# Optimization experiments

Measured on AMD Instinct MI355X. Metric: run time of the kernel, lower is better.

## Reference

```python
import jax, jax.numpy as jnp
import numpy as np

B, T, D = 8, 4096, 1024

def setup_inputs() -> dict:
    key = jax.random.key(0)
    ks = jax.random.split(key, 7)
    s1 = 1.0 / np.sqrt(D)
    return {
        "x":  jax.random.normal(ks[0], (B, T, D), dtype=jnp.float32),
        "W1": jax.random.normal(ks[1], (D, D), dtype=jnp.float32) * s1,   # attn_1.weight [out,in]
        "b1": jnp.zeros((D,), dtype=jnp.float32),
        "w2": jax.random.normal(ks[2], (1, D), dtype=jnp.float32) * s1,   # attn_2.weight [1,in]
        "b2": jnp.zeros((1,), dtype=jnp.float32),
        "Wc": jax.random.normal(ks[3], (D, 2 * D), dtype=jnp.float32) * (1.0 / np.sqrt(2 * D)),
        "bc": jnp.zeros((D,), dtype=jnp.float32),
    }

def reference(x, W1, b1, w2, b2, Wc, bc):
    # additive attention scores: [B, T, 1] -> [B, T]
    h = jnp.tanh(jnp.einsum('btd,ed->bte', x, W1) + b1)
    s = (jnp.einsum('btd,od->bto', h, w2) + b2)[..., 0]          # [B, T]
    # causal prefix softmax via cumulative sums (single O(T) pass).
    # softmax is shift-invariant, so subtracting the global per-batch max is stable.
    m = jnp.max(s, axis=1, keepdims=True)                        # [B, 1]
    e = jnp.exp(s - m)                                           # [B, T]
    num = jnp.cumsum(e[..., None] * x, axis=1)                   # [B, T, D]
    den = jnp.cumsum(e, axis=1)[..., None]                       # [B, T, 1]
    ctx = num / den                                              # [B, T, D]
    combined = jnp.concatenate((ctx, x), axis=2)                 # [B, T, 2D]
    out = jnp.tanh(jnp.einsum('btk,dk->btd', combined, Wc) + bc)
    return out
```

## Files before the change

### kernel.cpp

```cpp
#include <hip/hip_runtime.h>
#include <cmath>


#define Mtot 32768
#define Dd 1024
#define Tt 4096
#define Bb 8
#define NCHUNK 64
#define TCH 64

typedef __bf16 bf16x8 __attribute__((ext_vector_type(8)));
typedef float f32x4 __attribute__((ext_vector_type(4)));

__device__ __forceinline__ unsigned short f2bf(float f) {
  unsigned int u = __float_as_uint(f);
  unsigned int r = (u + 0x7FFFu + ((u >> 16) & 1u)) >> 16;
  return (unsigned short)r;
}
__device__ __forceinline__ float bf2f(unsigned short s) {
  return __uint_as_float(((unsigned int)s) << 16);
}

__device__ __forceinline__ void gload16(const unsigned short* g, unsigned short* l) {
  __builtin_amdgcn_global_load_lds(
      (const __attribute__((address_space(1))) unsigned int*)g,
      (__attribute__((address_space(3))) unsigned int*)l, 16, 0, 0);
}

__device__ __forceinline__ void mfma_core(
    const unsigned short* __restrict__ A0, const unsigned short* __restrict__ A1,
    const unsigned short* __restrict__ W, int ldw, int Ktot,
    int m0, int n0, unsigned short* As, unsigned short* Bs, f32x4 acc[4][4]) {
  int tid = threadIdx.x;
  int lane = tid & 63, w = tid >> 6;
  int wm = w >> 1, wn = w & 1;
  int quad = lane >> 4, c = lane & 15;
  int lrow = lane >> 3;
  int col8 = (lane & 7) ^ lrow;

  for (int k0 = 0; k0 < Ktot; k0 += 64) {
    const unsigned short* Asrc = (k0 < 1024) ? A0 : A1;
    int ka = k0 & 1023;
#pragma unroll
    for (int j = 0; j < 4; ++j) {
      int row = w * 32 + j * 8 + lrow;
      gload16(Asrc + (size_t)(m0 + row) * 1024 + ka + col8 * 8, As + w * 2048 + j * 512);
      gload16(W + (size_t)(n0 + row) * ldw + k0 + col8 * 8, Bs + w * 2048 + j * 512);
    }
    __syncthreads();
#pragma unroll
    for (int ks = 0; ks < 2; ++ks) {
      bf16x8 af[4], bfr[4];
#pragma unroll
      for (int i = 0; i < 4; ++i) {
        int ra = wm * 64 + i * 16 + c;
        int pa = (ks * 4 + quad) ^ (ra & 7);
        af[i] = *(const bf16x8*)(As + ra * 64 + pa * 8);
        int rb = wn * 64 + i * 16 + c;
        int pb = (ks * 4 + quad) ^ (rb & 7);
        bfr[i] = *(const bf16x8*)(Bs + rb * 64 + pb * 8);
      }
#pragma unroll
      for (int i = 0; i < 4; ++i)
#pragma unroll
        for (int jn = 0; jn < 4; ++jn)
          acc[i][jn] = __builtin_amdgcn_mfma_f32_16x16x32_bf16(af[i], bfr[jn], acc[i][jn], 0, 0, 0);
    }
    __syncthreads();
  }
}

__global__ __launch_bounds__(256) void gemm_s(
    const unsigned short* __restrict__ xb, const unsigned short* __restrict__ W1b,
    const float* __restrict__ b1, const float* __restrict__ w2, float* __restrict__ s) {
  __shared__ unsigned short As[128 * 64];
  __shared__ unsigned short Bs[128 * 64];
  f32x4 acc[4][4];
#pragma unroll
  for (int i = 0; i < 4; ++i)
#pragma unroll
    for (int j = 0; j < 4; ++j) acc[i][j] = (f32x4){0.f, 0.f, 0.f, 0.f};
  int m0 = blockIdx.x * 128, n0 = blockIdx.y * 128;
  mfma_core(xb, xb, W1b, 1024, 1024, m0, n0, As, Bs, acc);
  int tid = threadIdx.x, lane = tid & 63, w = tid >> 6;
  int wm = w >> 1, wn = w & 1, quad = lane >> 4, c = lane & 15;
#pragma unroll
  for (int i = 0; i < 4; ++i) {
#pragma unroll
    for (int r = 0; r < 4; ++r) {
      float p = 0.f;
#pragma unroll
      for (int jn = 0; jn < 4; ++jn) {
        int n = n0 + wn * 64 + jn * 16 + c;
        p += w2[n] * tanhf(acc[i][jn][r] + b1[n]);
      }
      p += __shfl_xor(p, 1, 64);
      p += __shfl_xor(p, 2, 64);
      p += __shfl_xor(p, 4, 64);
      p += __shfl_xor(p, 8, 64);
      if (c == 0) atomicAdd(&s[m0 + wm * 64 + i * 16 + quad * 4 + r], p);
    }
  }
}

__global__ __launch_bounds__(256) void gemm_out(
    const unsigned short* __restrict__ qb, const unsigned short* __restrict__ xb,
    const unsigned short* __restrict__ Wcb, const float* __restrict__ bc_,
    float* __restrict__ out) {
  __shared__ unsigned short As[128 * 64];
  __shared__ unsigned short Bs[128 * 64];
  f32x4 acc[4][4];
#pragma unroll
  for (int i = 0; i < 4; ++i)
#pragma unroll
    for (int j = 0; j < 4; ++j) acc[i][j] = (f32x4){0.f, 0.f, 0.f, 0.f};
  int m0 = blockIdx.x * 128, n0 = blockIdx.y * 128;
  mfma_core(qb, xb, Wcb, 2048, 2048, m0, n0, As, Bs, acc);
  int tid = threadIdx.x, lane = tid & 63, w = tid >> 6;
  int wm = w >> 1, wn = w & 1, quad = lane >> 4, c = lane & 15;
#pragma unroll
  for (int i = 0; i < 4; ++i)
#pragma unroll
    for (int jn = 0; jn < 4; ++jn) {
      int n = n0 + wn * 64 + jn * 16 + c;
      float bias = bc_[n];
#pragma unroll
      for (int r = 0; r < 4; ++r) {
        int m = m0 + wm * 64 + i * 16 + quad * 4 + r;
        out[(size_t)m * Dd + n] = tanhf(acc[i][jn][r] + bias);
      }
    }
}

__global__ __launch_bounds__(256) void cast_x(const float4* __restrict__ x,
                                              ushort4* __restrict__ xb) {
  int i = blockIdx.x * 256 + threadIdx.x;
  float4 v = x[i];
  ushort4 o;
  o.x = f2bf(v.x); o.y = f2bf(v.y); o.z = f2bf(v.z); o.w = f2bf(v.w);
  xb[i] = o;
}

__global__ __launch_bounds__(256) void cast_w(
    const float* __restrict__ W1, const float* __restrict__ Wc,
    ushort4* __restrict__ W1b, ushort4* __restrict__ Wcb) {
  int i = blockIdx.x * 256 + threadIdx.x;
  if (i < 262144) {
    float4 v = ((const float4*)W1)[i];
    ushort4 o;
    o.x = f2bf(v.x); o.y = f2bf(v.y); o.z = f2bf(v.z); o.w = f2bf(v.w);
    W1b[i] = o;
  } else {
    int p = i - 262144;
    float4 v = ((const float4*)Wc)[p];
    ushort4 o;
    o.x = f2bf(v.x); o.y = f2bf(v.y); o.z = f2bf(v.z); o.w = f2bf(v.w);
    Wcb[p] = o;
  }
}

__global__ __launch_bounds__(256) void softmax_scan(
    const float* __restrict__ s, float* __restrict__ e, float* __restrict__ den) {
  int b = blockIdx.x, tid = threadIdx.x;
  const float* sb = s + (size_t)b * Tt;
  __shared__ float wsum[4], woff[4], redm[4];
  __shared__ float carry_s, total_s;
  int lane = tid & 63, wid = tid >> 6;
  float m = -1e30f;
  for (int i = tid; i < Tt; i += 256) m = fmaxf(m, sb[i]);
#pragma unroll
  for (int off = 32; off > 0; off >>= 1) m = fmaxf(m, __shfl_down(m, off, 64));
  if (lane == 0) redm[wid] = m;
  __syncthreads();
  if (tid == 0) {
    float mm = redm[0];
    for (int w = 1; w < 4; ++w) mm = fmaxf(mm, redm[w]);
    redm[0] = mm;
    carry_s = 0.f;
  }
  __syncthreads();
  m = redm[0];
  for (int c = 0; c < 16; ++c) {
    int t = c * 256 + tid;
    float v = expf(sb[t] - m);
    e[(size_t)b * Tt + t] = v;
    float sc = v;
#pragma unroll
    for (int off = 1; off < 64; off <<= 1) {
      float tt = __shfl_up(sc, off, 64);
      if (lane >= off) sc += tt;
    }
    if (lane == 63) wsum[wid] = sc;
    __syncthreads();
    if (tid == 0) {
      float a = 0.f;
      for (int w = 0; w < 4; ++w) { woff[w] = a; a += wsum[w]; }
      total_s = a;
    }
    __syncthreads();
    den[(size_t)b * Tt + t] = sc + woff[wid] + carry_s;
    __syncthreads();
    if (tid == 0) carry_s += total_s;
    __syncthreads();
  }
}

__global__ __launch_bounds__(1024) void chunk_sums(
    const unsigned short* __restrict__ xb, const float* __restrict__ e,
    float* __restrict__ S) {
  int bc = blockIdx.x;
  int b = bc >> 6, c = bc & 63;
  int d = threadIdx.x;
  const unsigned short* xp = xb + ((size_t)(b * Tt + c * TCH)) * Dd + d;
  const float* eb = e + (size_t)b * Tt + c * TCH;
  float acc = 0.f;
#pragma unroll 8
  for (int t = 0; t < TCH; ++t) acc += eb[t] * bf2f(xp[(size_t)t * Dd]);
  S[((size_t)bc) * Dd + d] = acc;
}

__global__ __launch_bounds__(256) void chunk_prefix(float* __restrict__ S) {
  int idx = blockIdx.x * 256 + threadIdx.x;
  int b = idx >> 10, d = idx & 1023;
  float* Sb = S + (size_t)b * NCHUNK * Dd + d;
  float acc = 0.f;
#pragma unroll 8
  for (int c = 0; c < NCHUNK; ++c) {
    float t = Sb[(size_t)c * Dd];
    Sb[(size_t)c * Dd] = acc;
    acc += t;
  }
}

__global__ __launch_bounds__(1024) void scan_q(
    const unsigned short* __restrict__ xb, const float* __restrict__ e,
    const float* __restrict__ den, const float* __restrict__ S,
    unsigned short* __restrict__ qb) {
  int bc = blockIdx.x;
  int b = bc >> 6, c = bc & 63;
  int d = threadIdx.x;
  int tbase = b * Tt + c * TCH;
  float acc = S[((size_t)bc) * Dd + d];
  const unsigned short* xp = xb + (size_t)tbase * Dd + d;
  const float* eb = e + tbase;
  const float* db = den + tbase;
  unsigned short* qp = qb + (size_t)tbase * Dd + d;
#pragma unroll 4
  for (int t = 0; t < TCH; ++t) {
    acc += eb[t] * bf2f(xp[(size_t)t * Dd]);
    qp[(size_t)t * Dd] = f2bf(acc / db[t]);
  }
}

extern "C" void kernel_launch(void* const* d_in, const int* in_sizes, int n_in,
                              void* d_out, int out_size, void* d_ws, size_t ws_size,
                              hipStream_t stream) {
  const float* x  = (const float*)d_in[0];
  const float* W1 = (const float*)d_in[1];
  const float* b1 = (const float*)d_in[2];
  const float* w2 = (const float*)d_in[3];
  const float* Wc = (const float*)d_in[5];
  const float* bc = (const float*)d_in[6];
  float* out = (float*)d_out;

  float* ws = (float*)d_ws;
  float* s_buf   = ws;
  float* e_buf   = ws + 32768;
  float* den_buf = ws + 65536;
  float* S_buf   = ws + 98304;
  unsigned short* qb  = (unsigned short*)(ws + 622592);
  unsigned short* xb  = (unsigned short*)(ws + 17399808);
  unsigned short* W1b = (unsigned short*)(ws + 34177024);
  unsigned short* Wcb = (unsigned short*)(ws + 34701312);

  hipMemsetAsync(s_buf, 0, (size_t)Mtot * sizeof(float), stream);

  cast_x<<<32768, 256, 0, stream>>>((const float4*)x, (ushort4*)xb);
  cast_w<<<3072, 256, 0, stream>>>(W1, Wc, (ushort4*)W1b, (ushort4*)Wcb);

  gemm_s<<<dim3(Mtot / 128, Dd / 128), 256, 0, stream>>>(xb, W1b, b1, w2, s_buf);
  softmax_scan<<<Bb, 256, 0, stream>>>(s_buf, e_buf, den_buf);
  chunk_sums<<<Bb * NCHUNK, 1024, 0, stream>>>(xb, e_buf, S_buf);
  chunk_prefix<<<Bb * Dd / 256, 256, 0, stream>>>(S_buf);
  scan_q<<<Bb * NCHUNK, 1024, 0, stream>>>(xb, e_buf, den_buf, S_buf, qb);
  gemm_out<<<dim3(Mtot / 128, Dd / 128), 256, 0, stream>>>(qb, xb, Wcb, bc, out);
}
```

Measured before the change: 579.7 us.

## Fuse cast kernels with memset, use fast tanh, and register-resident softmax scan

```diff
diff --git a/kernel.cpp b/kernel.cpp
--- a/kernel.cpp
+++ b/kernel.cpp
@@ -19,6 +19,9 @@
 }
 __device__ __forceinline__ float bf2f(unsigned short s) {
   return __uint_as_float(((unsigned int)s) << 16);
+}
+__device__ __forceinline__ float tanh_fast(float x) {
+  return 1.0f - __fdividef(2.0f, __expf(2.0f * x) + 1.0f);
 }
 
 __device__ __forceinline__ void gload16(const unsigned short* g, unsigned short* l) {
@@ -92,7 +95,7 @@
 #pragma unroll
       for (int jn = 0; jn < 4; ++jn) {
         int n = n0 + wn * 64 + jn * 16 + c;
-        p += w2[n] * tanhf(acc[i][jn][r] + b1[n]);
+        p += w2[n] * tanh_fast(acc[i][jn][r] + b1[n]);
       }
       p += __shfl_xor(p, 1, 64);
       p += __shfl_xor(p, 2, 64);
@@ -127,81 +130,86 @@
 #pragma unroll
       for (int r = 0; r < 4; ++r) {
         int m = m0 + wm * 64 + i * 16 + quad * 4 + r;
-        out[(size_t)m * Dd + n] = tanhf(acc[i][jn][r] + bias);
+        out[(size_t)m * Dd + n] = tanh_fast(acc[i][jn][r] + bias);
       }
     }
 }
 
-__global__ __launch_bounds__(256) void cast_x(const float4* __restrict__ x,
-                                              ushort4* __restrict__ xb) {
+__global__ __launch_bounds__(256) void cast_all(
+    const float4* __restrict__ x, const float4* __restrict__ W1,
+    const float4* __restrict__ Wc, ushort4* __restrict__ xb,
+    ushort4* __restrict__ W1b, ushort4* __restrict__ Wcb,
+    float4* __restrict__ s) {
   int i = blockIdx.x * 256 + threadIdx.x;
-  float4 v = x[i];
-  ushort4 o;
-  o.x = f2bf(v.x); o.y = f2bf(v.y); o.z = f2bf(v.z); o.w = f2bf(v.w);
-  xb[i] = o;
-}
-
-__global__ __launch_bounds__(256) void cast_w(
-    const float* __restrict__ W1, const float* __restrict__ Wc,
-    ushort4* __restrict__ W1b, ushort4* __restrict__ Wcb) {
-  int i = blockIdx.x * 256 + threadIdx.x;
-  if (i < 262144) {
-    float4 v = ((const float4*)W1)[i];
+  if (i < 8388608) {
+    float4 v = x[i];
     ushort4 o;
     o.x = f2bf(v.x); o.y = f2bf(v.y); o.z = f2bf(v.z); o.w = f2bf(v.w);
-    W1b[i] = o;
-  } else {
-    int p = i - 262144;
-    float4 v = ((const float4*)Wc)[p];
+    xb[i] = o;
+  } else if (i < 8650752) {
+    int p = i - 8388608;
+    float4 v = W1[p];
+    ushort4 o;
+    o.x = f2bf(v.x); o.y = f2bf(v.y); o.z = f2bf(v.z); o.w = f2bf(v.w);
+    W1b[p] = o;
+  } else if (i < 9175040) {
+    int p = i - 8650752;
+    float4 v = Wc[p];
     ushort4 o;
     o.x = f2bf(v.x); o.y = f2bf(v.y); o.z = f2bf(v.z); o.w = f2bf(v.w);
     Wcb[p] = o;
+  } else {
+    s[i - 9175040] = (float4){0.f, 0.f, 0.f, 0.f};
   }
 }
 
 __global__ __launch_bounds__(256) void softmax_scan(
     const float* __restrict__ s, float* __restrict__ e, float* __restrict__ den) {
   int b = blockIdx.x, tid = threadIdx.x;
-  const float* sb = s + (size_t)b * Tt;
-  __shared__ float wsum[4], woff[4], redm[4];
-  __shared__ float carry_s, total_s;
   int lane = tid & 63, wid = tid >> 6;
-  float m = -1e30f;
-  for (int i = tid; i < Tt; i += 256) m = fmaxf(m, sb[i]);
-#pragma unroll
-  for (int off = 32; off > 0; off >>= 1) m = fmaxf(m, __shfl_down(m, off, 64));
+  __shared__ float redm[4], wsum[4];
+  const float4* sb4 = (const float4*)(s + (size_t)b * Tt);
+  float v[16];
+#pragma unroll
+  for (int j = 0; j < 4; ++j) {
+    float4 f = sb4[tid * 4 + j];
+    v[j * 4 + 0] = f.x; v[j * 4 + 1] = f.y; v[j * 4 + 2] = f.z; v[j * 4 + 3] = f.w;
+  }
+  float m = v[0];
+#pragma unroll
+  for (int j = 1; j < 16; ++j) m = fmaxf(m, v[j]);
+#pragma unroll
+  for (int off = 32; off > 0; off >>= 1) m = fmaxf(m, __shfl_xor(m, off, 64));
   if (lane == 0) redm[wid] = m;
   __syncthreads();
-  if (tid == 0) {
-    float mm = redm[0];
-    for (int w = 1; w < 4; ++w) mm = fmaxf(mm, redm[w]);
-    redm[0] = mm;
-    carry_s = 0.f;
-  }
+  m = fmaxf(fmaxf(redm[0], redm[1]), fmaxf(redm[2], redm[3]));
+  float ev[16];
+  float ls = 0.f;
+#pragma unroll
+  for (int j = 0; j < 16; ++j) { ev[j] = __expf(v[j] - m); ls += ev[j]; }
+  float sc = ls;
+#pragma unroll
+  for (int off = 1; off < 64; off <<= 1) {
+    float tt = __shfl_up(sc, off, 64);
+    if (lane >= off) sc += tt;
+  }
+  if (lane == 63) wsum[wid] = sc;
   __syncthreads();
-  m = redm[0];
-  for (int c = 0; c < 16; ++c) {
-    int t = c * 256 + tid;
-    float v = expf(sb[t] - m);
-    e[(size_t)b * Tt + t] = v;
-    float sc = v;
-#pragma unroll
-    for (int off = 1; off < 64; off <<= 1) {
-      float tt = __shfl_up(sc, off, 64);
-      if (lane >= off) sc += tt;
-    }
-    if (lane == 63) wsum[wid] = sc;
-    __syncthreads();
-    if (tid == 0) {
-      float a = 0.f;
-      for (int w = 0; w < 4; ++w) { woff[w] = a; a += wsum[w]; }
-      total_s = a;
-    }
-    __syncthreads();
-    den[(size_t)b * Tt + t] = sc + woff[wid] + carry_s;
-    __syncthreads();
-    if (tid == 0) carry_s += total_s;
-    __syncthreads();
+  float woff = 0.f;
+#pragma unroll
+  for (int w = 0; w < 4; ++w) woff += (w < wid) ? wsum[w] : 0.f;
+  float run = sc - ls + woff;
+  float4* eb4 = (float4*)(e + (size_t)b * Tt);
+  float4* db4 = (float4*)(den + (size_t)b * Tt);
+#pragma unroll
+  for (int j = 0; j < 4; ++j) {
+    float4 eo, doo;
+    run += ev[j * 4 + 0]; eo.x = ev[j * 4 + 0]; doo.x = run;
+    run += ev[j * 4 + 1]; eo.y = ev[j * 4 + 1]; doo.y = run;
+    run += ev[j * 4 + 2]; eo.z = ev[j * 4 + 2]; doo.z = run;
+    run += ev[j * 4 + 3]; eo.w = ev[j * 4 + 3]; doo.w = run;
+    eb4[tid * 4 + j] = eo;
+    db4[tid * 4 + j] = doo;
   }
 }
 
@@ -248,7 +256,7 @@
 #pragma unroll 4
   for (int t = 0; t < TCH; ++t) {
     acc += eb[t] * bf2f(xp[(size_t)t * Dd]);
-    qp[(size_t)t * Dd] = f2bf(acc / db[t]);
+    qp[(size_t)t * Dd] = f2bf(acc * __fdividef(1.0f, db[t]));
   }
 }
 
@@ -273,10 +281,10 @@
   unsigned short* W1b = (unsigned short*)(ws + 34177024);
   unsigned short* Wcb = (unsigned short*)(ws + 34701312);
 
-  hipMemsetAsync(s_buf, 0, (size_t)Mtot * sizeof(float), stream);
-
-  cast_x<<<32768, 256, 0, stream>>>((const float4*)x, (ushort4*)xb);
-  cast_w<<<3072, 256, 0, stream>>>(W1, Wc, (ushort4*)W1b, (ushort4*)Wcb);
+  cast_all<<<35872, 256, 0, stream>>>((const float4*)x, (const float4*)W1,
+                                      (const float4*)Wc, (ushort4*)xb,
+                                      (ushort4*)W1b, (ushort4*)Wcb,
+                                      (float4*)s_buf);
 
   gemm_s<<<dim3(Mtot / 128, Dd / 128), 256, 0, stream>>>(xb, W1b, b1, w2, s_buf);
   softmax_scan<<<Bb, 256, 0, stream>>>(s_buf, e_buf, den_buf);
```

After: 535.6 us. 1.08x faster.
